# Kernel tuning notes

Hardware: AMD Instinct MI355X
Metric: run time of the kernel (lower is better)

Reference implementation:

```python
import jax, jax.numpy as jnp
import numpy as np

VOCAB = 100000
EMBED = 64
SENT = 20
MEM = 50
BATCH = 32
HOPS = 3
PAD_ID = 0


def position_encoding(sentence_size, embedding_size):
    # Section 4.1 of MemN2N paper, vectorized. Returns [sentence_size, embedding_size].
    i = np.arange(1, embedding_size + 1, dtype=np.float32)[:, None]   # [E,1]
    j = np.arange(1, sentence_size + 1, dtype=np.float32)[None, :]    # [1,S]
    enc = (i - (embedding_size + 1) / 2.0) * (j - (sentence_size + 1) / 2.0)
    enc = 1.0 + 4.0 * enc / embedding_size / sentence_size
    enc[:, -1] = 1.0
    return jnp.asarray(enc.T, dtype=jnp.float32)  # [S,E]


def setup_inputs() -> dict:
    key = jax.random.key(0)
    k1, k2, k3, k4 = jax.random.split(key, 4)
    stories = jax.random.randint(k1, (BATCH, MEM, SENT), 0, VOCAB, dtype=jnp.int64 if jax.config.jax_enable_x64 else jnp.int32)
    queries = jax.random.randint(k2, (BATCH, SENT), 0, VOCAB, dtype=jnp.int64 if jax.config.jax_enable_x64 else jnp.int32)
    A = jax.random.normal(k3, (VOCAB, EMBED), dtype=jnp.float32) * 0.1
    C = jax.random.normal(k4, (HOPS, VOCAB, EMBED), dtype=jnp.float32) * 0.1
    # padding_idx=PAD_ID rows are zero, as in nn.Embedding(padding_idx=...)
    A = A.at[PAD_ID].set(0.0)
    C = C.at[:, PAD_ID].set(0.0)
    encoding = position_encoding(SENT, EMBED)
    return {"stories": stories, "queries": queries, "A": A, "C": C, "encoding": encoding}


def reference(stories, queries, A, C, encoding):
    # queries: [B,S], stories: [B,M,S], A: [V,E], C: [hops,V,E], encoding: [S,E]
    q_emb = A[queries]                                # [B,S,E]
    u = (q_emb * encoding).sum(axis=1)                # [B,E]
    for hop in range(HOPS):
        table_in = A if hop == 0 else C[hop - 1]
        emb_A = table_in[stories]                     # [B,M,S,E]
        m = (emb_A * encoding).sum(axis=2)            # [B,M,E]
        dotted = jnp.einsum('bme,be->bm', m, u)       # [B,M]
        probs = jax.nn.softmax(dotted, axis=-1)       # [B,M]
        emb_C = C[hop][stories]                       # [B,M,S,E]
        c = (emb_C * encoding).sum(axis=2)            # [B,M,E]
        o = jnp.einsum('bm,bme->be', probs, c)        # [B,E]
        u = u + o
    return u @ C[-1].T                                # [B,V]
```

## Files before the change

### kernel.cpp

```cpp
#include <hip/hip_runtime.h>
#include <hip/hip_bf16.h>

#define VOCAB 100000
#define EMBED 64
#define SENT  20
#define MEM   50
#define BATCH 32
#define HOPS  3

__device__ __forceinline__ float bfr(unsigned short x) {
    union { unsigned int u; float f; } cv;
    cv.u = ((unsigned int)x) << 16;
    return cv.f;
}

__device__ __forceinline__ bool is_bf16(const void* enc) {
    return ((const unsigned int*)enc)[639] == 0x3F803F80u;
}

__device__ __forceinline__ float loadT(const void* p, size_t idx, bool bf) {
    return bf ? bfr(((const unsigned short*)p)[idx]) : ((const float*)p)[idx];
}

__device__ __forceinline__ float wave_sum(float d) {
#pragma unroll
    for (int off = 32; off > 0; off >>= 1) d += __shfl_xor(d, off, 64);
    return d;
}

__global__ __launch_bounds__(1024) void k_recur(
    const int* __restrict__ stories,
    const int* __restrict__ queries,
    const void* __restrict__ A,
    const void* __restrict__ C,
    const void* __restrict__ enc,
    float* __restrict__ u3g)
{
    const bool bf = is_bf16(enc);
    const int b    = blockIdx.x;
    const int tid  = threadIdx.x;
    const int e    = tid & 63;
    const int widx = tid >> 6;

    __shared__ float cls[MEM][EMBED];
    __shared__ float dls[MEM];

    const size_t VE = (size_t)VOCAB * EMBED;

    float encr[SENT];
#pragma unroll
    for (int s = 0; s < SENT; ++s) encr[s] = loadT(enc, s * EMBED + e, bf);

    float u_e = 0.f;
    {
        int wq = (e < SENT) ? queries[b * SENT + e] : 0;
#pragma unroll
        for (int s = 0; s < SENT; ++s) {
            int w = __shfl(wq, s, 64);
            u_e += loadT(A, (size_t)w * EMBED + e, bf) * encr[s];
        }
    }

    for (int hop = 0; hop < HOPS; ++hop) {
        const void* Tin   = (hop == 0) ? A : C;
        const size_t toff = (hop == 2) ? VE : 0;
        const size_t coff = (size_t)hop * VE;

        for (int mm = widx; mm < MEM; mm += 16) {
            int wst = (e < SENT) ? stories[(b * MEM + mm) * SENT + e] : 0;
            float macc = 0.f, cacc = 0.f;
#pragma unroll
            for (int s = 0; s < SENT; ++s) {
                int w = __shfl(wst, s, 64);
                size_t ro = (size_t)w * EMBED + e;
                macc += loadT(Tin, toff + ro, bf) * encr[s];
                cacc += loadT(C, coff + ro, bf) * encr[s];
            }
            cls[mm][e] = cacc;
            float d = wave_sum(macc * u_e);
            if (e == 0) dls[mm] = d;
        }
        __syncthreads();

        float x = (e < MEM) ? dls[e] : -3.4e38f;
        float mx = x;
#pragma unroll
        for (int off = 32; off > 0; off >>= 1) mx = fmaxf(mx, __shfl_xor(mx, off, 64));
        float ex = (e < MEM) ? __expf(x - mx) : 0.f;
        float sm = wave_sum(ex);
        float p = ex / sm;
        float o = 0.f;
#pragma unroll
        for (int mm = 0; mm < MEM; ++mm)
            o += __shfl(p, mm, 64) * cls[mm][e];
        u_e += o;
        __syncthreads();
    }

    if (widx == 0) u3g[b * EMBED + e] = u_e;
}

__global__ __launch_bounds__(256) void k_out(const float* __restrict__ u,
                                             const void* __restrict__ Cbase,
                                             const void* __restrict__ enc,
                                             void* __restrict__ out)
{
    bool bf = is_bf16(enc);
    const size_t c2_off = (size_t)2 * VOCAB * EMBED;
    __shared__ __align__(16) float su[BATCH * EMBED];
    for (int i = threadIdx.x; i < BATCH * EMBED; i += 256) su[i] = u[i];
    __syncthreads();
    int v = blockIdx.x * 256 + threadIdx.x;
    if (v >= VOCAB) return;

    float row[EMBED];
    if (bf) {
        const uint4* rp = (const uint4*)((const unsigned short*)Cbase + c2_off + (size_t)v * EMBED);
#pragma unroll
        for (int i = 0; i < 8; ++i) {
            uint4 r = rp[i];
            row[i*8 + 0] = bfr((unsigned short)(r.x & 0xffff));
            row[i*8 + 1] = bfr((unsigned short)(r.x >> 16));
            row[i*8 + 2] = bfr((unsigned short)(r.y & 0xffff));
            row[i*8 + 3] = bfr((unsigned short)(r.y >> 16));
            row[i*8 + 4] = bfr((unsigned short)(r.z & 0xffff));
            row[i*8 + 5] = bfr((unsigned short)(r.z >> 16));
            row[i*8 + 6] = bfr((unsigned short)(r.w & 0xffff));
            row[i*8 + 7] = bfr((unsigned short)(r.w >> 16));
        }
    } else {
        const float4* rp = (const float4*)((const float*)Cbase + c2_off + (size_t)v * EMBED);
#pragma unroll
        for (int i = 0; i < 16; ++i) {
            float4 r = rp[i];
            row[i*4 + 0] = r.x; row[i*4 + 1] = r.y;
            row[i*4 + 2] = r.z; row[i*4 + 3] = r.w;
        }
    }

    float res[BATCH];
#pragma unroll
    for (int bb = 0; bb < BATCH; ++bb) {
        const float4* sp = (const float4*)(su + bb * EMBED);
        float acc = 0.f;
#pragma unroll
        for (int e4 = 0; e4 < 16; ++e4) {
            float4 us = sp[e4];
            acc += row[e4*4+0]*us.x + row[e4*4+1]*us.y
                 + row[e4*4+2]*us.z + row[e4*4+3]*us.w;
        }
        res[bb] = acc;
    }

    if (bf) {
        unsigned short* ob = (unsigned short*)out;
#pragma unroll
        for (int bb = 0; bb < BATCH; ++bb) {
            __hip_bfloat16 h = __float2bfloat16(res[bb]);
            ob[(size_t)bb * VOCAB + v] = *(unsigned short*)&h;
        }
    } else {
        float* of = (float*)out;
#pragma unroll
        for (int bb = 0; bb < BATCH; ++bb)
            of[(size_t)bb * VOCAB + v] = res[bb];
    }
}

extern "C" void kernel_launch(void* const* d_in, const int* in_sizes, int n_in,
                              void* d_out, int out_size, void* d_ws, size_t ws_size,
                              hipStream_t stream)
{
    const int*  stories = (const int*)d_in[0];
    const int*  queries = (const int*)d_in[1];
    const void* A       = d_in[2];
    const void* C       = d_in[3];
    const void* enc     = d_in[4];
    float*      u3g     = (float*)d_ws;

    k_recur<<<BATCH, 1024, 0, stream>>>(stories, queries, A, C, enc, u3g);
    k_out<<<(VOCAB + 255) / 256, 256, 0, stream>>>(u3g, C, enc, d_out);
}
```

Before: 192.7 us.

## Split recurrence into wide gather kernel and small per-batch hop kernel

Hoists the embedding gathers for all hops out of the sequential recurrence into a separate kernel that uses one wave per (hop, batch, memory) slot, spreading the work over about 1200 blocks instead of 32. A small 64-thread kernel per batch then does the dot products, softmax and weighted sum, reading the precomputed m and c vectors from workspace. The intent is to remove the latency-bound gather from a 32-block launch and fill the GPU. The cost is an extra launch and a round trip of the m and c tensors through global memory.

```diff
diff --git a/kernel.cpp b/kernel.cpp
--- a/kernel.cpp
+++ b/kernel.cpp
@@ -8,6 +8,8 @@
 #define BATCH 32
 #define HOPS  3
 
+#define NSLOT (HOPS * BATCH * MEM)
+
 __device__ __forceinline__ float bfr(unsigned short x) {
     union { unsigned int u; float f; } cv;
     cv.u = ((unsigned int)x) << 16;
@@ -28,76 +30,99 @@
     return d;
 }
 
-__global__ __launch_bounds__(1024) void k_recur(
+__global__ __launch_bounds__(256) void k_gather(
     const int* __restrict__ stories,
     const int* __restrict__ queries,
     const void* __restrict__ A,
     const void* __restrict__ C,
     const void* __restrict__ enc,
-    float* __restrict__ u3g)
+    float* __restrict__ m_ws,
+    float* __restrict__ c_ws,
+    float* __restrict__ u0g)
 {
     const bool bf = is_bf16(enc);
-    const int b    = blockIdx.x;
     const int tid  = threadIdx.x;
     const int e    = tid & 63;
-    const int widx = tid >> 6;
-
-    __shared__ float cls[MEM][EMBED];
-    __shared__ float dls[MEM];
-
+    const int gw   = blockIdx.x * 4 + (tid >> 6);
     const size_t VE = (size_t)VOCAB * EMBED;
 
     float encr[SENT];
 #pragma unroll
     for (int s = 0; s < SENT; ++s) encr[s] = loadT(enc, s * EMBED + e, bf);
 
-    float u_e = 0.f;
-    {
-        int wq = (e < SENT) ? queries[b * SENT + e] : 0;
-#pragma unroll
-        for (int s = 0; s < SENT; ++s) {
-            int w = __shfl(wq, s, 64);
-            u_e += loadT(A, (size_t)w * EMBED + e, bf) * encr[s];
-        }
-    }
-
-    for (int hop = 0; hop < HOPS; ++hop) {
+    if (gw < NSLOT) {
+        const int hop = gw / (BATCH * MEM);
+        const int bm  = gw % (BATCH * MEM);
         const void* Tin   = (hop == 0) ? A : C;
         const size_t toff = (hop == 2) ? VE : 0;
         const size_t coff = (size_t)hop * VE;
 
-        for (int mm = widx; mm < MEM; mm += 16) {
-            int wst = (e < SENT) ? stories[(b * MEM + mm) * SENT + e] : 0;
-            float macc = 0.f, cacc = 0.f;
-#pragma unroll
-            for (int s = 0; s < SENT; ++s) {
-                int w = __shfl(wst, s, 64);
-                size_t ro = (size_t)w * EMBED + e;
-                macc += loadT(Tin, toff + ro, bf) * encr[s];
-                cacc += loadT(C, coff + ro, bf) * encr[s];
+        int wst = (e < SENT) ? stories[bm * SENT + e] : 0;
+        float macc = 0.f, cacc = 0.f;
+#pragma unroll
+        for (int s = 0; s < SENT; ++s) {
+            int w = __shfl(wst, s, 64);
+            size_t ro = (size_t)w * EMBED + e;
+            macc += loadT(Tin, toff + ro, bf) * encr[s];
+            cacc += loadT(C, coff + ro, bf) * encr[s];
+        }
+        m_ws[gw * EMBED + e] = macc;
+        c_ws[gw * EMBED + e] = cacc;
+    } else if (gw < NSLOT + BATCH) {
+        const int b = gw - NSLOT;
+        int wq = (e < SENT) ? queries[b * SENT + e] : 0;
+        float u = 0.f;
+#pragma unroll
+        for (int s = 0; s < SENT; ++s) {
+            int w = __shfl(wq, s, 64);
+            u += loadT(A, (size_t)w * EMBED + e, bf) * encr[s];
+        }
+        u0g[b * EMBED + e] = u;
+    }
+}
+
+__global__ __launch_bounds__(64) void k_recur2(
+    const float* __restrict__ m_ws,
+    const float* __restrict__ c_ws,
+    const float* __restrict__ u0g,
+    float* __restrict__ u3g)
+{
+    const int b = blockIdx.x;
+    const int e = threadIdx.x;
+
+    float u = u0g[b * EMBED + e];
+
+    for (int hop = 0; hop < HOPS; ++hop) {
+        const size_t base = ((size_t)hop * BATCH * MEM + b * MEM) * EMBED;
+
+        float dval = -3.4e38f;
+#pragma unroll
+        for (int g = 0; g < MEM; g += 10) {
+            float mv[10];
+#pragma unroll
+            for (int k = 0; k < 10; ++k)
+                mv[k] = m_ws[base + (g + k) * EMBED + e];
+#pragma unroll
+            for (int k = 0; k < 10; ++k) {
+                float d = wave_sum(mv[k] * u);
+                if (e == g + k) dval = d;
             }
-            cls[mm][e] = cacc;
-            float d = wave_sum(macc * u_e);
-            if (e == 0) dls[mm] = d;
-        }
-        __syncthreads();
-
-        float x = (e < MEM) ? dls[e] : -3.4e38f;
-        float mx = x;
+        }
+
+        float mx = dval;
 #pragma unroll
         for (int off = 32; off > 0; off >>= 1) mx = fmaxf(mx, __shfl_xor(mx, off, 64));
-        float ex = (e < MEM) ? __expf(x - mx) : 0.f;
+        float ex = (e < MEM) ? __expf(dval - mx) : 0.f;
         float sm = wave_sum(ex);
         float p = ex / sm;
+
         float o = 0.f;
 #pragma unroll
         for (int mm = 0; mm < MEM; ++mm)
-            o += __shfl(p, mm, 64) * cls[mm][e];
-        u_e += o;
-        __syncthreads();
-    }
-
-    if (widx == 0) u3g[b * EMBED + e] = u_e;
+            o += __shfl(p, mm, 64) * c_ws[base + mm * EMBED + e];
+        u += o;
+    }
+    u3g[b * EMBED + e] = u;
 }
 
 __global__ __launch_bounds__(256) void k_out(const float* __restrict__ u,
@@ -176,8 +201,16 @@
     const void* A       = d_in[2];
     const void* C       = d_in[3];
     const void* enc     = d_in[4];
-    float*      u3g     = (float*)d_ws;
-
-    k_recur<<<BATCH, 1024, 0, stream>>>(stories, queries, A, C, enc, u3g);
+
+    float* m_ws = (float*)d_ws;
+    float* c_ws = m_ws + NSLOT * EMBED;
+    float* u0g  = c_ws + NSLOT * EMBED;
+    float* u3g  = u0g + BATCH * EMBED;
+
+    const int nwaves  = NSLOT + BATCH;
+    const int nblocks = (nwaves + 3) / 4;
+
+    k_gather<<<nblocks, 256, 0, stream>>>(stories, queries, A, C, enc, m_ws, c_ws, u0g);
+    k_recur2<<<BATCH, 64, 0, stream>>>(m_ws, c_ws, u0g, u3g);
     k_out<<<(VOCAB + 255) / 256, 256, 0, stream>>>(u3g, C, enc, d_out);
 }
```

Measured after the change: 183.4 us. -4.9%, faster.

## Split embedding gathers into a wide parallel kernel before the hop recurrence

Applied to the files above, without the earlier changes.

The memory-hop recurrence previously ran on only 32 blocks, each gathering all story embeddings serially across hops. The gathers are now moved into a separate kernel that spreads every (table, batch, memory slot) position-encoded sum across ~1600 blocks, and each of the four distinct tables is gathered once instead of twice. A small recurrence kernel then loads the precomputed vectors into shared memory and does only the dot products, softmax and weighted sums. This costs an extra launch and a workspace round trip in exchange for far more memory-level parallelism.

```diff
diff --git a/kernel.cpp b/kernel.cpp
--- a/kernel.cpp
+++ b/kernel.cpp
@@ -8,6 +8,9 @@
 #define BATCH 32
 #define HOPS  3
 
+#define NSET  4
+#define NSLOT (NSET * BATCH * MEM)
+
 __device__ __forceinline__ float bfr(unsigned short x) {
     union { unsigned int u; float f; } cv;
     cv.u = ((unsigned int)x) << 16;
@@ -28,76 +31,111 @@
     return d;
 }
 
-__global__ __launch_bounds__(1024) void k_recur(
+__global__ __launch_bounds__(256) void k_gather(
     const int* __restrict__ stories,
     const int* __restrict__ queries,
     const void* __restrict__ A,
     const void* __restrict__ C,
     const void* __restrict__ enc,
+    float* __restrict__ mc_ws,
+    float* __restrict__ u0g)
+{
+    const bool bf = is_bf16(enc);
+    const int tid = threadIdx.x;
+    const int e   = tid & 63;
+    const int gw  = blockIdx.x * 4 + (tid >> 6);
+    const size_t VE = (size_t)VOCAB * EMBED;
+
+    float encr[SENT];
+#pragma unroll
+    for (int s = 0; s < SENT; ++s) encr[s] = loadT(enc, s * EMBED + e, bf);
+
+    if (gw < NSLOT) {
+        const int t  = gw / (BATCH * MEM);
+        const int bm = gw % (BATCH * MEM);
+        const void* T   = (t == 0) ? A : C;
+        const size_t to = (t == 0) ? 0 : (size_t)(t - 1) * VE;
+
+        int wst = (e < SENT) ? stories[bm * SENT + e] : 0;
+        float acc = 0.f;
+#pragma unroll
+        for (int s = 0; s < SENT; ++s) {
+            int w = __shfl(wst, s, 64);
+            acc += loadT(T, to + (size_t)w * EMBED + e, bf) * encr[s];
+        }
+        mc_ws[gw * EMBED + e] = acc;
+    } else if (gw < NSLOT + BATCH) {
+        const int b = gw - NSLOT;
+        int wq = (e < SENT) ? queries[b * SENT + e] : 0;
+        float u = 0.f;
+#pragma unroll
+        for (int s = 0; s < SENT; ++s) {
+            int w = __shfl(wq, s, 64);
+            u += loadT(A, (size_t)w * EMBED + e, bf) * encr[s];
+        }
+        u0g[b * EMBED + e] = u;
+    }
+}
+
+__global__ __launch_bounds__(256) void k_recur2(
+    const float* __restrict__ mc_ws,
+    const float* __restrict__ u0g,
     float* __restrict__ u3g)
 {
-    const bool bf = is_bf16(enc);
     const int b    = blockIdx.x;
     const int tid  = threadIdx.x;
-    const int e    = tid & 63;
+    const int lane = tid & 63;
     const int widx = tid >> 6;
 
-    __shared__ float cls[MEM][EMBED];
-    __shared__ float dls[MEM];
-
-    const size_t VE = (size_t)VOCAB * EMBED;
-
-    float encr[SENT];
-#pragma unroll
-    for (int s = 0; s < SENT; ++s) encr[s] = loadT(enc, s * EMBED + e, bf);
-
-    float u_e = 0.f;
-    {
-        int wq = (e < SENT) ? queries[b * SENT + e] : 0;
-#pragma unroll
-        for (int s = 0; s < SENT; ++s) {
-            int w = __shfl(wq, s, 64);
-            u_e += loadT(A, (size_t)w * EMBED + e, bf) * encr[s];
-        }
-    }
+    __shared__ float mc[NSET][MEM][65];
+    __shared__ float uls[EMBED];
+    __shared__ float ols[4][EMBED];
+
+    for (int idx = tid; idx < NSET * MEM * 16; idx += 256) {
+        int t  = idx / (MEM * 16);
+        int r  = idx % (MEM * 16);
+        int mm = r >> 4;
+        int e4 = r & 15;
+        const float4 v = *(const float4*)(mc_ws +
+            (((size_t)t * BATCH * MEM) + (size_t)b * MEM + mm) * EMBED + e4 * 4);
+        mc[t][mm][e4 * 4 + 0] = v.x;
+        mc[t][mm][e4 * 4 + 1] = v.y;
+        mc[t][mm][e4 * 4 + 2] = v.z;
+        mc[t][mm][e4 * 4 + 3] = v.w;
+    }
+    if (tid < EMBED) uls[tid] = u0g[b * EMBED + tid];
+    __syncthreads();
 
     for (int hop = 0; hop < HOPS; ++hop) {
-        const void* Tin   = (hop == 0) ? A : C;
-        const size_t toff = (hop == 2) ? VE : 0;
-        const size_t coff = (size_t)hop * VE;
-
-        for (int mm = widx; mm < MEM; mm += 16) {
-            int wst = (e < SENT) ? stories[(b * MEM + mm) * SENT + e] : 0;
-            float macc = 0.f, cacc = 0.f;
-#pragma unroll
-            for (int s = 0; s < SENT; ++s) {
-                int w = __shfl(wst, s, 64);
-                size_t ro = (size_t)w * EMBED + e;
-                macc += loadT(Tin, toff + ro, bf) * encr[s];
-                cacc += loadT(C, coff + ro, bf) * encr[s];
-            }
-            cls[mm][e] = cacc;
-            float d = wave_sum(macc * u_e);
-            if (e == 0) dls[mm] = d;
-        }
-        __syncthreads();
-
-        float x = (e < MEM) ? dls[e] : -3.4e38f;
+        float d = 0.f;
+        if (lane < MEM) {
+#pragma unroll
+            for (int e = 0; e < EMBED; ++e)
+                d += mc[hop][lane][e] * uls[e];
+        }
+        float x = (lane < MEM) ? d : -3.4e38f;
         float mx = x;
 #pragma unroll
         for (int off = 32; off > 0; off >>= 1) mx = fmaxf(mx, __shfl_xor(mx, off, 64));
-        float ex = (e < MEM) ? __expf(x - mx) : 0.f;
+        float ex = (lane < MEM) ? __expf(x - mx) : 0.f;
         float sm = wave_sum(ex);
         float p = ex / sm;
+
         float o = 0.f;
 #pragma unroll
-        for (int mm = 0; mm < MEM; ++mm)
-            o += __shfl(p, mm, 64) * cls[mm][e];
-        u_e += o;
+        for (int k = 0; k < 13; ++k) {
+            int mm = widx * 13 + k;
+            if (mm < MEM)
+                o += __shfl(p, mm, 64) * mc[hop + 1][mm][lane];
+        }
+        ols[widx][lane] = o;
         __syncthreads();
-    }
-
-    if (widx == 0) u3g[b * EMBED + e] = u_e;
+        if (tid < EMBED)
+            uls[tid] += ols[0][tid] + ols[1][tid] + ols[2][tid] + ols[3][tid];
+        __syncthreads();
+    }
+
+    if (tid < EMBED) u3g[b * EMBED + tid] = uls[tid];
 }
 
 __global__ __launch_bounds__(256) void k_out(const float* __restrict__ u,
@@ -176,8 +214,15 @@
     const void* A       = d_in[2];
     const void* C       = d_in[3];
     const void* enc     = d_in[4];
-    float*      u3g     = (float*)d_ws;
-
-    k_recur<<<BATCH, 1024, 0, stream>>>(stories, queries, A, C, enc, u3g);
+
+    float* mc_ws = (float*)d_ws;
+    float* u0g   = mc_ws + NSLOT * EMBED;
+    float* u3g   = u0g + BATCH * EMBED;
+
+    const int nwaves  = NSLOT + BATCH;
+    const int nblocks = (nwaves + 3) / 4;
+
+    k_gather<<<nblocks, 256, 0, stream>>>(stories, queries, A, C, enc, mc_ws, u0g);
+    k_recur2<<<BATCH, 256, 0, stream>>>(mc_ws, u0g, u3g);
     k_out<<<(VOCAB + 255) / 256, 256, 0, stream>>>(u3g, C, enc, d_out);
 }
```

Measured after the change: 159.4 us. 17.3% less time.
